# Kernel optimization log

Hardware: AMD Instinct MI355X
Metric: run time of the kernel (lower is better)

Reference implementation:

```python
import jax, jax.numpy as jnp
import numpy as np

N, E, D_IN, HID, HEADS, D_OUT, R = 20000, 640000, 256, 128, 4, 128, 32
NEG_SLOPE = 0.2  # PyG GATConv default


def setup_inputs() -> dict:
    key = jax.random.key(0)
    ks = jax.random.split(key, 12)
    s = 0.05
    return {
        "x": jax.random.normal(ks[0], (N, D_IN), jnp.float32),
        "edge_index": jax.random.randint(ks[1], (2, E), 0, N, dtype=jnp.int64),
        "edge_type": jax.random.randint(ks[2], (E,), 0, R, dtype=jnp.int64),
        "rel_emb": jax.random.normal(ks[3], (R, D_IN), jnp.float32) * s,
        "W1": jax.random.normal(ks[4], (D_IN, HEADS * HID), jnp.float32) * s,
        "att_src1": jax.random.normal(ks[5], (HEADS, HID), jnp.float32) * s,
        "att_dst1": jax.random.normal(ks[6], (HEADS, HID), jnp.float32) * s,
        "b1": jnp.zeros((HEADS * HID,), jnp.float32),
        "W2": jax.random.normal(ks[7], (HEADS * HID, D_OUT), jnp.float32) * s,
        "att_src2": jax.random.normal(ks[8], (1, D_OUT), jnp.float32) * s,
        "att_dst2": jax.random.normal(ks[9], (1, D_OUT), jnp.float32) * s,
        "b2": jnp.zeros((D_OUT,), jnp.float32),
    }


def _gat_conv(x, src, dst, W, a_src, a_dst, bias, heads, ch):
    """PyG GATConv (eval mode, self loops already in src/dst)."""
    n = x.shape[0]
    h = (x @ W).reshape(n, heads, ch)                      # [N,H,C]
    alpha_s = jnp.einsum('nhc,hc->nh', h, a_src)           # [N,H]
    alpha_d = jnp.einsum('nhc,hc->nh', h, a_dst)
    e = jax.nn.leaky_relu(alpha_s[src] + alpha_d[dst], NEG_SLOPE)  # [E,H]
    # segment softmax over incoming edges of each dst node
    m = jax.ops.segment_max(e, dst, num_segments=n)        # [N,H]
    p = jnp.exp(e - m[dst])
    denom = jax.ops.segment_sum(p, dst, num_segments=n)
    alpha = p / (denom[dst] + 1e-16)                       # [E,H]
    out = jax.ops.segment_sum(h[src] * alpha[:, :, None], dst, num_segments=n)
    return out.reshape(n, heads * ch) + bias


def reference(x, edge_index, edge_type, rel_emb, W1, att_src1, att_dst1, b1,
              W2, att_src2, att_dst2, b2):
    src, dst = edge_index[0], edge_index[1]
    # relational feature injection: x_mod[src] += rel_emb[edge_type]
    x_mod = x.at[src].add(rel_emb[edge_type])
    # GATConv adds self loops by default
    loop = jnp.arange(N, dtype=src.dtype)
    s2 = jnp.concatenate([src, loop])
    d2 = jnp.concatenate([dst, loop])
    h = _gat_conv(x_mod, s2, d2, W1, att_src1, att_dst1, b1, HEADS, HID)
    h = jax.nn.elu(h)
    return _gat_conv(h, s2, d2, W2, att_src2, att_dst2, b2, 1, D_OUT)
```

## Files before the change

### kernel.cpp

```cpp
#include <hip/hip_runtime.h>


#define D_IN   256
#define HID1   512
#define NHEADS 4
#define DOUT   128
#define NREL   32
#define NEG_SLOPE 0.2f
#define M_PAD  20096
#define NB     128

static __device__ __forceinline__ unsigned short f2b(float f) {
  union { float f; unsigned int i; } v; v.f = f;
  unsigned int x = v.i;
  return (unsigned short)((x + 0x7fffu + ((x >> 16) & 1u)) >> 16);
}
static __device__ __forceinline__ float lrelu(float x) {
  return x > 0.f ? x : NEG_SLOPE * x;
}

typedef __attribute__((ext_vector_type(8))) short bf16x8;
typedef __attribute__((ext_vector_type(4))) float f32x4;
typedef __attribute__((ext_vector_type(2))) float f32x2;

static __device__ __forceinline__ f32x2 up2(unsigned int u) {
  union { unsigned int i; float f; } lo, hi;
  lo.i = u << 16; hi.i = u & 0xffff0000u;
  f32x2 v; v.x = lo.f; v.y = hi.f; return v;
}
static __device__ __forceinline__ void pkfma(f32x2& a, f32x2 b, f32x2 c) {
  asm("v_pk_fma_f32 %0, %1, %2, %0" : "+v"(a) : "v"(b), "v"(c));
}
static __device__ __forceinline__ void accp(f32x2* acc, float w, uint4 r) {
  f32x2 wv = (f32x2)(w);
  pkfma(acc[0], wv, up2(r.x));
  pkfma(acc[1], wv, up2(r.y));
  pkfma(acc[2], wv, up2(r.z));
  pkfma(acc[3], wv, up2(r.w));
}

__global__ __launch_bounds__(256) void hist_prep_kernel(
    const int* __restrict__ src, const int* __restrict__ dst,
    const int* __restrict__ et, unsigned int* __restrict__ counts8,
    int* __restrict__ gtable, int E, int n, int cb,
    const float* __restrict__ W1, const float* __restrict__ W2,
    unsigned short* __restrict__ W1T, unsigned short* __restrict__ W2T,
    const float* __restrict__ att_s1, const float* __restrict__ att_d1,
    float* __restrict__ us4, float* __restrict__ ud4,
    const float* __restrict__ att_s2, const float* __restrict__ att_d2,
    float* __restrict__ vs, float* __restrict__ vd) {
  int b = blockIdx.x;
  int t = threadIdx.x;
  if (b < NB) {
    extern __shared__ int hist[];
    for (int i = t; i < n; i += 256) hist[i] = 0;
    __syncthreads();
    int per = (E + NB - 1) / NB;
    int e0 = b * per;
    int e1 = min(e0 + per, E);
    for (int e = e0 + t; e < e1; e += 256) {
      atomicAdd(&hist[dst[e]], 1);
      int s = src[e], r = et[e];
      atomicAdd(&counts8[(size_t)s * 8 + (r >> 2)], 1u << (8 * (r & 3)));
    }
    __syncthreads();
    for (int i = t; i < n; i += 256) gtable[(size_t)b * n + i] = hist[i];
  } else if (b < NB + cb) {
    int idx = (b - NB) * 256 + t;
    if (idx < D_IN * HID1) {
      int r = idx / HID1, c = idx % HID1;
      W1T[(size_t)c * D_IN + r] = f2b(W1[idx]);
    } else {
      int k = idx - D_IN * HID1;
      if (k < HID1 * DOUT) {
        int r = k / DOUT, c = k % DOUT;
        W2T[(size_t)c * HID1 + r] = f2b(W2[k]);
      }
    }
  } else if (b == NB + cb) {
    int k = t;
    float us[4] = {0.f, 0.f, 0.f, 0.f}, ud[4] = {0.f, 0.f, 0.f, 0.f};
    for (int h = 0; h < 4; ++h)
      for (int c = 0; c < 128; ++c) {
        float wv = W1[(size_t)k * HID1 + h * 128 + c];
        us[h] += wv * att_s1[h * 128 + c];
        ud[h] += wv * att_d1[h * 128 + c];
      }
    ((float4*)us4)[k] = make_float4(us[0], us[1], us[2], us[3]);
    ((float4*)ud4)[k] = make_float4(ud[0], ud[1], ud[2], ud[3]);
  } else {
#pragma unroll
    for (int rr = 0; rr < 2; ++rr) {
      int r = t * 2 + rr;
      float ss = 0.f, dd = 0.f;
      for (int c = 0; c < DOUT; ++c) {
        float wv = W2[(size_t)r * DOUT + c];
        ss += wv * att_s2[c];
        dd += wv * att_d2[c];
      }
      vs[r] = ss; vd[r] = dd;
    }
  }
}

__global__ void colsum_kernel(const int* __restrict__ gtable,
                              int* __restrict__ deg, int n) {
  int d = blockIdx.x * 256 + threadIdx.x;
  if (d >= n) return;
  int s = 0;
#pragma unroll 8
  for (int b = 0; b < NB; ++b) s += gtable[(size_t)b * n + d];
  deg[d] = s;
}

__global__ void scan_local(const int* __restrict__ in, int* __restrict__ out,
                           int* __restrict__ bsum, int n) {
  __shared__ int wsum[4];
  int t = threadIdx.x;
  int base = blockIdx.x * 1024 + t * 4;
  int v0 = (base + 0 < n) ? in[base + 0] : 0;
  int v1 = (base + 1 < n) ? in[base + 1] : 0;
  int v2 = (base + 2 < n) ? in[base + 2] : 0;
  int v3 = (base + 3 < n) ? in[base + 3] : 0;
  int s = v0 + v1 + v2 + v3;
  int lane = t & 63, w = t >> 6;
  int sc = s;
  for (int off = 1; off < 64; off <<= 1) {
    int u = __shfl_up(sc, off);
    if (lane >= off) sc += u;
  }
  if (lane == 63) wsum[w] = sc;
  __syncthreads();
  int woff = 0;
  for (int i = 0; i < w; ++i) woff += wsum[i];
  int excl = woff + sc - s;
  if (base + 0 < n) out[base + 0] = excl;
  if (base + 1 < n) out[base + 1] = excl + v0;
  if (base + 2 < n) out[base + 2] = excl + v0 + v1;
  if (base + 3 < n) out[base + 3] = excl + v0 + v1 + v2;
  if (t == 255) bsum[blockIdx.x] = woff + sc;
}

__global__ void scan_blocks(int* __restrict__ bsum, int nb,
                            int* __restrict__ offsets, int n) {
  int t = threadIdx.x;
  int v = (t < nb) ? bsum[t] : 0;
  int sc = v;
  for (int off = 1; off < 64; off <<= 1) {
    int u = __shfl_up(sc, off);
    if (t >= off) sc += u;
  }
  if (t < nb) bsum[t] = sc - v;
  if (t == nb - 1) offsets[n] = v;
}

__global__ void rebase_kernel(int* __restrict__ gtable,
                              const int* __restrict__ offsets,
                              const int* __restrict__ bsum, int n) {
  int d = blockIdx.x * 256 + threadIdx.x;
  if (d >= n) return;
  int run = offsets[d] + bsum[d >> 10];
#pragma unroll 8
  for (int b = 0; b < NB; ++b) {
    size_t idx = (size_t)b * n + d;
    int v = gtable[idx];
    gtable[idx] = run;
    run += v;
  }
}

__global__ __launch_bounds__(256) void scatter2_kernel(
    const int* __restrict__ src, const int* __restrict__ dst,
    const int* __restrict__ gtable, int* __restrict__ csr_src,
    uint2* __restrict__ wexp,
    const float* __restrict__ as1, const float* __restrict__ ad1,
    int E, int n) {
  extern __shared__ int cur[];
  int b = blockIdx.x;
  int t = threadIdx.x;
  for (int i = t; i < n; i += 256) cur[i] = gtable[(size_t)b * n + i];
  __syncthreads();
  int per = (E + NB - 1) / NB;
  int e0 = b * per;
  int e1 = min(e0 + per, E);
  for (int e = e0 + t; e < e1; e += 256) {
    int d = dst[e], s = src[e];
    int pos = atomicAdd(&cur[d], 1);
    csr_src[pos] = s;
    float4 av = ((const float4*)as1)[s];
    float4 dv = ((const float4*)ad1)[d];
    unsigned short h0 = f2b(__expf(lrelu(av.x + dv.x)));
    unsigned short h1 = f2b(__expf(lrelu(av.y + dv.y)));
    unsigned short h2 = f2b(__expf(lrelu(av.z + dv.z)));
    unsigned short h3 = f2b(__expf(lrelu(av.w + dv.w)));
    wexp[pos] = make_uint2((unsigned)h0 | ((unsigned)h1 << 16),
                           (unsigned)h2 | ((unsigned)h3 << 16));
  }
}

__global__ __launch_bounds__(256) void xmod_kernel(
    const float* __restrict__ x, const unsigned int* __restrict__ counts8,
    const float* __restrict__ rel, const float* __restrict__ us4,
    const float* __restrict__ ud4, unsigned short* __restrict__ x_modb,
    float* __restrict__ as1, float* __restrict__ ad1, int n_nodes) {
  int wv = threadIdx.x >> 6;
  int node = blockIdx.x * 4 + wv;
  if (node >= n_nodes) return;
  int l = threadIdx.x & 63;
  int r5 = l & 31;
  unsigned int cw = counts8[(size_t)node * 8 + (r5 >> 2)];
  int cnt_l = (int)((cw >> (8 * (r5 & 3))) & 0xffu);
  const float4* x4 = (const float4*)x;
  const float4* rel4 = (const float4*)rel;
  float4 v = x4[(size_t)node * 64 + l];
#pragma unroll
  for (int r = 0; r < NREL; ++r) {
    int c = __shfl(cnt_l, r);
    if (c) {
      float4 rv = rel4[r * 64 + l];
      float fc = (float)c;
      v.x += fc * rv.x; v.y += fc * rv.y; v.z += fc * rv.z; v.w += fc * rv.w;
    }
  }
  ushort4 o;
  o.x = f2b(v.x); o.y = f2b(v.y); o.z = f2b(v.z); o.w = f2b(v.w);
  *(ushort4*)(x_modb + (size_t)node * D_IN + l * 4) = o;
  const float4* usv = (const float4*)us4;
  const float4* udv = (const float4*)ud4;
  float vv[4] = {v.x, v.y, v.z, v.w};
  float sh[4] = {0.f, 0.f, 0.f, 0.f}, dh[4] = {0.f, 0.f, 0.f, 0.f};
#pragma unroll
  for (int i = 0; i < 4; ++i) {
    float4 uu = usv[l * 4 + i];
    float4 dd = udv[l * 4 + i];
    sh[0] += vv[i] * uu.x; sh[1] += vv[i] * uu.y; sh[2] += vv[i] * uu.z; sh[3] += vv[i] * uu.w;
    dh[0] += vv[i] * dd.x; dh[1] += vv[i] * dd.y; dh[2] += vv[i] * dd.z; dh[3] += vv[i] * dd.w;
  }
  for (int off = 32; off; off >>= 1) {
#pragma unroll
    for (int h = 0; h < 4; ++h) {
      sh[h] += __shfl_xor(sh[h], off);
      dh[h] += __shfl_xor(dh[h], off);
    }
  }
  if (l == 0) {
    ((float4*)as1)[node] = make_float4(sh[0], sh[1], sh[2], sh[3]);
    ((float4*)ad1)[node] = make_float4(dh[0], dh[1], dh[2], dh[3]);
  }
}

__global__ __launch_bounds__(256) void aggregate1_kernel(
    const unsigned short* __restrict__ x_modb,
    const uint2* __restrict__ wexp,
    const float* __restrict__ as1, const float* __restrict__ ad1,
    const int* __restrict__ offsets, const int* __restrict__ bsum,
    const int* __restrict__ csr_src,
    unsigned short* __restrict__ agg_xb, int n_nodes) {
  int node = blockIdx.x * 4 + (threadIdx.x >> 6);
  if (node >= n_nodes) return;
  int lane = threadIdx.x & 63;
  int half = lane >> 5, l32 = lane & 31;
  int lo = offsets[node] + bsum[node >> 10];
  int hi = offsets[node + 1] + bsum[(node + 1) >> 10];
  const uint4* xv = (const uint4*)x_modb;

  f32x2 acc[4][4];
#pragma unroll
  for (int h = 0; h < 4; ++h)
#pragma unroll
    for (int k = 0; k < 4; ++k) acc[h][k] = (f32x2)(0.f);
  f32x2 den01 = (f32x2)(0.f), den23 = (f32x2)(0.f);

  int j = lo + half;
  int s = (j < hi) ? csr_src[j] : node;
  uint2 w = (j < hi) ? wexp[j] : make_uint2(0u, 0u);
  uint4 r = xv[(unsigned)((s << 5) | l32)];
  while (j < hi) {
    int jn = j + 2;
    int sn = (jn < hi) ? csr_src[jn] : node;
    uint2 wn = (jn < hi) ? wexp[jn] : make_uint2(0u, 0u);
    uint4 rn = xv[(unsigned)((sn << 5) | l32)];
    f32x2 w01 = up2(w.x), w23 = up2(w.y);
    den01 += w01; den23 += w23;
    f32x2 x0 = up2(r.x), x1 = up2(r.y), x2 = up2(r.z), x3 = up2(r.w);
    f32x2 wv0 = (f32x2)(w01.x), wv1 = (f32x2)(w01.y);
    f32x2 wv2 = (f32x2)(w23.x), wv3 = (f32x2)(w23.y);
    pkfma(acc[0][0], wv0, x0); pkfma(acc[0][1], wv0, x1);
    pkfma(acc[0][2], wv0, x2); pkfma(acc[0][3], wv0, x3);
    pkfma(acc[1][0], wv1, x0); pkfma(acc[1][1], wv1, x1);
    pkfma(acc[1][2], wv1, x2); pkfma(acc[1][3], wv1, x3);
    pkfma(acc[2][0], wv2, x0); pkfma(acc[2][1], wv2, x1);
    pkfma(acc[2][2], wv2, x2); pkfma(acc[2][3], wv2, x3);
    pkfma(acc[3][0], wv3, x0); pkfma(acc[3][1], wv3, x1);
    pkfma(acc[3][2], wv3, x2); pkfma(acc[3][3], wv3, x3);
    j = jn; s = sn; w = wn; r = rn;
  }
  if (half == 0) {
    float4 av = ((const float4*)as1)[node];
    float4 dv = ((const float4*)ad1)[node];
    unsigned short h0 = f2b(__expf(lrelu(av.x + dv.x)));
    unsigned short h1 = f2b(__expf(lrelu(av.y + dv.y)));
    unsigned short h2 = f2b(__expf(lrelu(av.z + dv.z)));
    unsigned short h3 = f2b(__expf(lrelu(av.w + dv.w)));
    unsigned wlo = (unsigned)h0 | ((unsigned)h1 << 16);
    unsigned whi = (unsigned)h2 | ((unsigned)h3 << 16);
    f32x2 w01 = up2(wlo), w23 = up2(whi);
    den01 += w01; den23 += w23;
    uint4 rs = xv[(unsigned)((node << 5) | l32)];
    f32x2 x0 = up2(rs.x), x1 = up2(rs.y), x2 = up2(rs.z), x3 = up2(rs.w);
    f32x2 wv0 = (f32x2)(w01.x), wv1 = (f32x2)(w01.y);
    f32x2 wv2 = (f32x2)(w23.x), wv3 = (f32x2)(w23.y);
    pkfma(acc[0][0], wv0, x0); pkfma(acc[0][1], wv0, x1);
    pkfma(acc[0][2], wv0, x2); pkfma(acc[0][3], wv0, x3);
    pkfma(acc[1][0], wv1, x0); pkfma(acc[1][1], wv1, x1);
    pkfma(acc[1][2], wv1, x2); pkfma(acc[1][3], wv1, x3);
    pkfma(acc[2][0], wv2, x0); pkfma(acc[2][1], wv2, x1);
    pkfma(acc[2][2], wv2, x2); pkfma(acc[2][3], wv2, x3);
    pkfma(acc[3][0], wv3, x0); pkfma(acc[3][1], wv3, x1);
    pkfma(acc[3][2], wv3, x2); pkfma(acc[3][3], wv3, x3);
  }
#pragma unroll
  for (int h = 0; h < 4; ++h)
#pragma unroll
    for (int k = 0; k < 4; ++k) {
      acc[h][k].x += __shfl_xor(acc[h][k].x, 32);
      acc[h][k].y += __shfl_xor(acc[h][k].y, 32);
    }
  den01.x += __shfl_xor(den01.x, 32); den01.y += __shfl_xor(den01.y, 32);
  den23.x += __shfl_xor(den23.x, 32); den23.y += __shfl_xor(den23.y, 32);
  if (half == 0) {
    float inv[4];
    inv[0] = 1.f / (den01.x + 1e-16f);
    inv[1] = 1.f / (den01.y + 1e-16f);
    inv[2] = 1.f / (den23.x + 1e-16f);
    inv[3] = 1.f / (den23.y + 1e-16f);
#pragma unroll
    for (int h = 0; h < 4; ++h) {
      uint4 o;
      o.x = (unsigned)f2b(acc[h][0].x * inv[h]) | ((unsigned)f2b(acc[h][0].y * inv[h]) << 16);
      o.y = (unsigned)f2b(acc[h][1].x * inv[h]) | ((unsigned)f2b(acc[h][1].y * inv[h]) << 16);
      o.z = (unsigned)f2b(acc[h][2].x * inv[h]) | ((unsigned)f2b(acc[h][2].y * inv[h]) << 16);
      o.w = (unsigned)f2b(acc[h][3].x * inv[h]) | ((unsigned)f2b(acc[h][3].y * inv[h]) << 16);
      *(uint4*)(agg_xb + ((size_t)h * M_PAD + node) * D_IN + l32 * 8) = o;
    }
  }
}

template <int BM, int MODE>
__global__ __launch_bounds__(256) void mfma_gemm(
    const unsigned short* __restrict__ A, const unsigned short* __restrict__ BT,
    unsigned short* __restrict__ C, int M, int N, int K,
    const float* __restrict__ bias, const float* __restrict__ vs,
    const float* __restrict__ vd, float* __restrict__ as2, float* __restrict__ ad2) {
  constexpr int MFR = BM / 32;
  __shared__ __align__(16) unsigned short Asl[BM * 32];
  __shared__ __align__(16) unsigned short Bsl[128 * 32];
  int tid = threadIdx.x;
  int m0 = blockIdx.y * BM, n0 = blockIdx.x * 128;
  int lane = tid & 63, wv = tid >> 6;
  int wm = wv & 1, wn = wv >> 1;
  int l16 = lane & 15, quad = lane >> 4;
  int lr = lane >> 2, lseg = lane & 3;
  if (MODE == 1) A += (size_t)blockIdx.x * M_PAD * K;

  f32x4 acc[MFR][4];
#pragma unroll
  for (int i = 0; i < MFR; ++i)
#pragma unroll
    for (int j = 0; j < 4; ++j) acc[i][j] = (f32x4)(0.f);

  for (int k0 = 0; k0 < K; k0 += 32) {
#pragma unroll
    for (int c = wv; c < BM / 16; c += 4) {
      int gr = m0 + c * 16 + lr; gr = gr < M ? gr : M - 1;
      __builtin_amdgcn_global_load_lds(
          (const __attribute__((address_space(1))) void*)(A + (size_t)gr * K + k0 + lseg * 8),
          (__attribute__((address_space(3))) void*)(&Asl[c * 512]), 16, 0, 0);
    }
#pragma unroll
    for (int c = wv; c < 8; c += 4) {
      int gr = n0 + c * 16 + lr;
      __builtin_amdgcn_global_load_lds(
          (const __attribute__((address_space(1))) void*)(BT + (size_t)gr * K + k0 + lseg * 8),
          (__attribute__((address_space(3))) void*)(&Bsl[c * 512]), 16, 0, 0);
    }
    __syncthreads();
    bf16x8 af[MFR], bfr[4];
#pragma unroll
    for (int mf = 0; mf < MFR; ++mf)
      af[mf] = *(const bf16x8*)(&Asl[(wm * (BM / 2) + mf * 16 + l16) * 32 + quad * 8]);
#pragma unroll
    for (int nf = 0; nf < 4; ++nf)
      bfr[nf] = *(const bf16x8*)(&Bsl[(wn * 64 + nf * 16 + l16) * 32 + quad * 8]);
#pragma unroll
    for (int mf = 0; mf < MFR; ++mf)
#pragma unroll
      for (int nf = 0; nf < 4; ++nf)
        acc[mf][nf] = __builtin_amdgcn_mfma_f32_16x16x32_bf16(af[mf], bfr[nf], acc[mf][nf], 0, 0, 0);
    __syncthreads();
  }
  if (MODE == 0) {
#pragma unroll
    for (int mf = 0; mf < MFR; ++mf)
#pragma unroll
      for (int nf = 0; nf < 4; ++nf)
#pragma unroll
        for (int r = 0; r < 4; ++r) {
          int row = m0 + wm * (BM / 2) + mf * 16 + quad * 4 + r;
          int col = n0 + wn * 64 + nf * 16 + l16;
          C[(size_t)row * N + col] = f2b(acc[mf][nf][r]);
        }
  } else {
#pragma unroll
    for (int mf = 0; mf < MFR; ++mf)
#pragma unroll
      for (int r = 0; r < 4; ++r) {
        int row = m0 + wm * (BM / 2) + mf * 16 + quad * 4 + r;
        float sd = 0.f, dd = 0.f;
#pragma unroll
        for (int nf = 0; nf < 4; ++nf) {
          int col = n0 + wn * 64 + nf * 16 + l16;
          float cv = acc[mf][nf][r] + bias[col];
          cv = cv > 0.f ? cv : expm1f(cv);
          C[(size_t)row * N + col] = f2b(cv);
          sd += cv * vs[col];
          dd += cv * vd[col];
        }
#pragma unroll
        for (int off = 1; off < 16; off <<= 1) {
          sd += __shfl_xor(sd, off);
          dd += __shfl_xor(dd, off);
        }
        if (l16 == 0 && row < M) {
          atomicAdd(&as2[row], sd);
          atomicAdd(&ad2[row], dd);
        }
      }
  }
}

__global__ __launch_bounds__(256) void aggregate2_kernel(
    const unsigned short* __restrict__ t2b,
    const float* __restrict__ as2, const float* __restrict__ ad2,
    const int* __restrict__ offsets, const int* __restrict__ bsum,
    const int* __restrict__ csr_src,
    const float* __restrict__ bias, float* __restrict__ out, int n_nodes) {
  int node = blockIdx.x * 4 + (threadIdx.x >> 6);
  if (node >= n_nodes) return;
  int lane = threadIdx.x & 63;
  int g = lane >> 4, l16 = lane & 15;
  int lo = offsets[node] + bsum[node >> 10];
  int hi = offsets[node + 1] + bsum[(node + 1) >> 10];
  float ad = ad2[node];

  const uint4* t2v = (const uint4*)t2b;
  f32x2 acc[4];
#pragma unroll
  for (int k = 0; k < 4; ++k) acc[k] = (f32x2)(0.f);
  float denom = 0.f;
  int nit = (hi - lo + 3) >> 2;
  int j = lo + g;
  bool valid = j < hi;
  int s = valid ? csr_src[j] : node;
  float asv = as2[s];
  uint4 tv = t2v[(unsigned)((s << 4) | l16)];
  for (int i = 0; i < nit; ++i) {
    int jn = j + 4;
    bool vn = jn < hi;
    int sn = vn ? csr_src[jn] : node;
    float asv_n = as2[sn];
    uint4 tvn = t2v[(unsigned)((sn << 4) | l16)];
    float w = valid ? __expf(lrelu(asv + ad)) : 0.f;
    accp(acc, w, tv);
    denom += w;
    j = jn; valid = vn; s = sn; asv = asv_n; tv = tvn;
  }
  if (g == 0) {
    uint4 tv2 = t2v[(unsigned)((node << 4) | l16)];
    float w = __expf(lrelu(as2[node] + ad));
    accp(acc, w, tv2);
    denom += w;
  }
#pragma unroll
  for (int k = 0; k < 4; ++k) {
    acc[k].x += __shfl_xor(acc[k].x, 16); acc[k].y += __shfl_xor(acc[k].y, 16);
    acc[k].x += __shfl_xor(acc[k].x, 32); acc[k].y += __shfl_xor(acc[k].y, 32);
  }
  denom += __shfl_xor(denom, 16);
  denom += __shfl_xor(denom, 32);
  if (g == 0) {
    float inv = 1.f / (denom + 1e-16f);
    float4 o0, o1;
    o0.x = acc[0].x * inv + bias[l16 * 8 + 0];
    o0.y = acc[0].y * inv + bias[l16 * 8 + 1];
    o0.z = acc[1].x * inv + bias[l16 * 8 + 2];
    o0.w = acc[1].y * inv + bias[l16 * 8 + 3];
    o1.x = acc[2].x * inv + bias[l16 * 8 + 4];
    o1.y = acc[2].y * inv + bias[l16 * 8 + 5];
    o1.z = acc[3].x * inv + bias[l16 * 8 + 6];
    o1.w = acc[3].y * inv + bias[l16 * 8 + 7];
    *(float4*)(out + (size_t)node * DOUT + l16 * 8) = o0;
    *(float4*)(out + (size_t)node * DOUT + l16 * 8 + 4) = o1;
  }
}

extern "C" void kernel_launch(void* const* d_in, const int* in_sizes, int n_in,
                              void* d_out, int out_size, void* d_ws, size_t ws_size,
                              hipStream_t stream) {
  const float* x     = (const float*)d_in[0];
  const int* ei      = (const int*)d_in[1];
  const int* etype   = (const int*)d_in[2];
  const float* rel   = (const float*)d_in[3];
  const float* W1    = (const float*)d_in[4];
  const float* at_s1 = (const float*)d_in[5];
  const float* at_d1 = (const float*)d_in[6];
  const float* b1    = (const float*)d_in[7];
  const float* W2    = (const float*)d_in[8];
  const float* at_s2 = (const float*)d_in[9];
  const float* at_d2 = (const float*)d_in[10];
  const float* b2v   = (const float*)d_in[11];
  float* out         = (float*)d_out;

  const int N = in_sizes[0] / D_IN;
  const int E = in_sizes[2];
  const int* srcv = ei;
  const int* dstv = ei + E;

  char* p = (char*)d_ws;
  auto carve = [&](size_t bytes) -> char* {
    char* r = p; p += (bytes + 255) & ~(size_t)255; return r;
  };
  unsigned int* counts8 = (unsigned int*)carve((size_t)N * 8 * 4);
  float* as2     = (float*)carve((size_t)N * 4);
  float* ad2     = (float*)carve((size_t)N * 4);
  size_t zero_bytes = (size_t)(p - (char*)counts8);
  int*   deg     = (int*)carve((size_t)N * 4);
  int*   offsets = (int*)carve(((size_t)N + 1) * 4);
  int*   bsum    = (int*)carve(64 * 4);
  float* as1     = (float*)carve((size_t)N * NHEADS * 4);
  float* ad1     = (float*)carve((size_t)N * NHEADS * 4);
  float* vs      = (float*)carve((size_t)HID1 * 4);
  float* vd      = (float*)carve((size_t)HID1 * 4);
  float* us4     = (float*)carve((size_t)D_IN * 4 * 4);
  float* ud4     = (float*)carve((size_t)D_IN * 4 * 4);
  int*   csr_src = (int*)carve((size_t)E * 4);
  uint2* wexp    = (uint2*)carve((size_t)E * 8);
  unsigned short* W1T    = (unsigned short*)carve((size_t)HID1 * D_IN * 2);
  unsigned short* W2T    = (unsigned short*)carve((size_t)DOUT * HID1 * 2);
  unsigned short* x_modb = (unsigned short*)carve((size_t)N * D_IN * 2);
  unsigned short* agg_xb = (unsigned short*)carve((size_t)NHEADS * M_PAD * D_IN * 2);
  unsigned short* h2b    = (unsigned short*)carve((size_t)M_PAD * HID1 * 2);
  unsigned short* t2b    = (unsigned short*)carve((size_t)M_PAD * DOUT * 2);
  int* gtable = (int*)h2b;

  (void)hipMemsetAsync(counts8, 0, zero_bytes, stream);

  int cb = (D_IN * HID1 + HID1 * DOUT + 255) / 256;
  int nb = (N + 1023) / 1024;
  int ldsb = N * 4;
  hist_prep_kernel<<<NB + cb + 2, 256, ldsb, stream>>>(
      srcv, dstv, etype, counts8, gtable, E, N, cb,
      W1, W2, W1T, W2T, at_s1, at_d1, us4, ud4, at_s2, at_d2, vs, vd);
  colsum_kernel<<<(N + 255) / 256, 256, 0, stream>>>(gtable, deg, N);
  scan_local<<<nb, 256, 0, stream>>>(deg, offsets, bsum, N);
  scan_blocks<<<1, 64, 0, stream>>>(bsum, nb, offsets, N);
  rebase_kernel<<<(N + 255) / 256, 256, 0, stream>>>(gtable, offsets, bsum, N);
  xmod_kernel<<<(N + 3) / 4, 256, 0, stream>>>(x, counts8, rel, us4, ud4, x_modb, as1, ad1, N);
  scatter2_kernel<<<NB, 256, ldsb, stream>>>(srcv, dstv, gtable, csr_src, wexp,
                                             as1, ad1, E, N);
  aggregate1_kernel<<<(N + 3) / 4, 256, 0, stream>>>(x_modb, wexp, as1, ad1, offsets,
                                                     bsum, csr_src, agg_xb, N);
  mfma_gemm<128, 1><<<dim3(NHEADS, M_PAD / 128), 256, 0, stream>>>(
      agg_xb, W1T, h2b, N, HID1, D_IN, b1, vs, vd, as2, ad2);
  mfma_gemm<64, 0><<<dim3(DOUT / 128, M_PAD / 64), 256, 0, stream>>>(
      h2b, W2T, t2b, N, DOUT, HID1, nullptr, nullptr, nullptr, nullptr, nullptr);
  aggregate2_kernel<<<(N + 3) / 4, 256, 0, stream>>>(
      t2b, as2, ad2, offsets, bsum, csr_src, b2v, out, N);
}
```

Before: 309.2 us.

## Fuse colsum with xmod, single-block scan, parallelize prep dots, fp32 edge weights

Parallelizes the attention-vector precompute blocks across more blocks with vectorized loads and shuffle reduction. Merges the degree column-sum into the x_mod kernel launch and replaces the three-kernel scan with a single-block serial scan, which removes the bsum indirection from the aggregators. Edge softmax weights are stored as fp32 float4 instead of packed bf16, and aggregate1 is unrolled two edges deep using op_sel packed FMAs. The result is fewer launches and less unpacking, at the cost of doubled edge-weight traffic and a serial single-block scan over 20k entries.

```diff
diff --git a/kernel.cpp b/kernel.cpp
--- a/kernel.cpp
+++ b/kernel.cpp
@@ -31,12 +31,35 @@
 static __device__ __forceinline__ void pkfma(f32x2& a, f32x2 b, f32x2 c) {
   asm("v_pk_fma_f32 %0, %1, %2, %0" : "+v"(a) : "v"(b), "v"(c));
 }
+static __device__ __forceinline__ void pkfma_l(f32x2& a, f32x2 b, f32x2 c) {
+  asm("v_pk_fma_f32 %0, %1, %2, %0 op_sel_hi:[0,1,1]"
+      : "+v"(a) : "v"(b), "v"(c));
+}
+static __device__ __forceinline__ void pkfma_h(f32x2& a, f32x2 b, f32x2 c) {
+  asm("v_pk_fma_f32 %0, %1, %2, %0 op_sel:[1,0,0]"
+      : "+v"(a) : "v"(b), "v"(c));
+}
 static __device__ __forceinline__ void accp(f32x2* acc, float w, uint4 r) {
   f32x2 wv = (f32x2)(w);
   pkfma(acc[0], wv, up2(r.x));
   pkfma(acc[1], wv, up2(r.y));
   pkfma(acc[2], wv, up2(r.z));
   pkfma(acc[3], wv, up2(r.w));
+}
+static __device__ __forceinline__ void acc4w(f32x2 acc[4][4], f32x2& den01,
+                                             f32x2& den23, float4 w, uint4 r) {
+  f32x2 w01; w01.x = w.x; w01.y = w.y;
+  f32x2 w23; w23.x = w.z; w23.y = w.w;
+  den01 += w01; den23 += w23;
+  f32x2 x0 = up2(r.x), x1 = up2(r.y), x2 = up2(r.z), x3 = up2(r.w);
+  pkfma_l(acc[0][0], w01, x0); pkfma_l(acc[0][1], w01, x1);
+  pkfma_l(acc[0][2], w01, x2); pkfma_l(acc[0][3], w01, x3);
+  pkfma_h(acc[1][0], w01, x0); pkfma_h(acc[1][1], w01, x1);
+  pkfma_h(acc[1][2], w01, x2); pkfma_h(acc[1][3], w01, x3);
+  pkfma_l(acc[2][0], w23, x0); pkfma_l(acc[2][1], w23, x1);
+  pkfma_l(acc[2][2], w23, x2); pkfma_l(acc[2][3], w23, x3);
+  pkfma_h(acc[3][0], w23, x0); pkfma_h(acc[3][1], w23, x1);
+  pkfma_h(acc[3][2], w23, x2); pkfma_h(acc[3][3], w23, x3);
 }
 
 __global__ __launch_bounds__(256) void hist_prep_kernel(
@@ -77,90 +100,137 @@
         W2T[(size_t)c * HID1 + r] = f2b(W2[k]);
       }
     }
-  } else if (b == NB + cb) {
-    int k = t;
-    float us[4] = {0.f, 0.f, 0.f, 0.f}, ud[4] = {0.f, 0.f, 0.f, 0.f};
-    for (int h = 0; h < 4; ++h)
-      for (int c = 0; c < 128; ++c) {
-        float wv = W1[(size_t)k * HID1 + h * 128 + c];
-        us[h] += wv * att_s1[h * 128 + c];
-        ud[h] += wv * att_d1[h * 128 + c];
-      }
-    ((float4*)us4)[k] = make_float4(us[0], us[1], us[2], us[3]);
-    ((float4*)ud4)[k] = make_float4(ud[0], ud[1], ud[2], ud[3]);
+  } else if (b < NB + cb + 8) {
+    int k = (b - NB - cb) * 32 + (t >> 3);
+    int ch0 = (t & 7) * 64;
+    int h = (t & 7) >> 1;
+    const float4* w4 = (const float4*)(W1 + (size_t)k * HID1 + ch0);
+    const float4* s4 = (const float4*)(att_s1 + ch0);
+    const float4* d4 = (const float4*)(att_d1 + ch0);
+    float us = 0.f, ud = 0.f;
+#pragma unroll
+    for (int i = 0; i < 16; ++i) {
+      float4 wv = w4[i], sv = s4[i], dv = d4[i];
+      us += wv.x * sv.x + wv.y * sv.y + wv.z * sv.z + wv.w * sv.w;
+      ud += wv.x * dv.x + wv.y * dv.y + wv.z * dv.z + wv.w * dv.w;
+    }
+    us += __shfl_xor(us, 1);
+    ud += __shfl_xor(ud, 1);
+    if ((t & 1) == 0) { us4[k * 4 + h] = us; ud4[k * 4 + h] = ud; }
   } else {
-#pragma unroll
-    for (int rr = 0; rr < 2; ++rr) {
-      int r = t * 2 + rr;
-      float ss = 0.f, dd = 0.f;
-      for (int c = 0; c < DOUT; ++c) {
-        float wv = W2[(size_t)r * DOUT + c];
-        ss += wv * att_s2[c];
-        dd += wv * att_d2[c];
-      }
-      vs[r] = ss; vd[r] = dd;
-    }
-  }
-}
-
-__global__ void colsum_kernel(const int* __restrict__ gtable,
-                              int* __restrict__ deg, int n) {
+    int r = (b - NB - cb - 8) * 128 + (t >> 1);
+    int c0 = (t & 1) * 64;
+    const float4* w4 = (const float4*)(W2 + (size_t)r * DOUT + c0);
+    const float4* s4 = (const float4*)(att_s2 + c0);
+    const float4* d4 = (const float4*)(att_d2 + c0);
+    float ss = 0.f, dd = 0.f;
+#pragma unroll
+    for (int i = 0; i < 16; ++i) {
+      float4 wv = w4[i], sv = s4[i], dv = d4[i];
+      ss += wv.x * sv.x + wv.y * sv.y + wv.z * sv.z + wv.w * sv.w;
+      dd += wv.x * dv.x + wv.y * dv.y + wv.z * dv.z + wv.w * dv.w;
+    }
+    ss += __shfl_xor(ss, 1);
+    dd += __shfl_xor(dd, 1);
+    if ((t & 1) == 0) { vs[r] = ss; vd[r] = dd; }
+  }
+}
+
+__global__ __launch_bounds__(256) void colsum_xmod_kernel(
+    const int* __restrict__ gtable, int* __restrict__ offsets, int cs,
+    const float* __restrict__ x, const unsigned int* __restrict__ counts8,
+    const float* __restrict__ rel, const float* __restrict__ us4,
+    const float* __restrict__ ud4, unsigned short* __restrict__ x_modb,
+    float* __restrict__ as1, float* __restrict__ ad1, int n_nodes) {
+  int b = blockIdx.x;
+  int t = threadIdx.x;
+  if (b < cs) {
+    int d = b * 256 + t;
+    if (d >= n_nodes) return;
+    int s = 0;
+    for (int bb = 0; bb < NB; ++bb) s += gtable[(size_t)bb * n_nodes + d];
+    offsets[d] = s;
+    return;
+  }
+  int wv = t >> 6;
+  int node = (b - cs) * 4 + wv;
+  if (node >= n_nodes) return;
+  int l = t & 63;
+  int r5 = l & 31;
+  unsigned int cw = counts8[(size_t)node * 8 + (r5 >> 2)];
+  int cnt_l = (int)((cw >> (8 * (r5 & 3))) & 0xffu);
+  const float4* x4 = (const float4*)x;
+  const float4* rel4 = (const float4*)rel;
+  float4 v = x4[(size_t)node * 64 + l];
+#pragma unroll
+  for (int r = 0; r < NREL; ++r) {
+    int c = __shfl(cnt_l, r);
+    if (c) {
+      float4 rv = rel4[r * 64 + l];
+      float fc = (float)c;
+      v.x += fc * rv.x; v.y += fc * rv.y; v.z += fc * rv.z; v.w += fc * rv.w;
+    }
+  }
+  ushort4 o;
+  o.x = f2b(v.x); o.y = f2b(v.y); o.z = f2b(v.z); o.w = f2b(v.w);
+  *(ushort4*)(x_modb + (size_t)node * D_IN + l * 4) = o;
+  const float4* usv = (const float4*)us4;
+  const float4* udv = (const float4*)ud4;
+  float vv[4] = {v.x, v.y, v.z, v.w};
+  float sh[4] = {0.f, 0.f, 0.f, 0.f}, dh[4] = {0.f, 0.f, 0.f, 0.f};
+#pragma unroll
+  for (int i = 0; i < 4; ++i) {
+    float4 uu = usv[l * 4 + i];
+    float4 dd = udv[l * 4 + i];
+    sh[0] += vv[i] * uu.x; sh[1] += vv[i] * uu.y; sh[2] += vv[i] * uu.z; sh[3] += vv[i] * uu.w;
+    dh[0] += vv[i] * dd.x; dh[1] += vv[i] * dd.y; dh[2] += vv[i] * dd.z; dh[3] += vv[i] * dd.w;
+  }
+  for (int off = 32; off; off >>= 1) {
+#pragma unroll
+    for (int h = 0; h < 4; ++h) {
+      sh[h] += __shfl_xor(sh[h], off);
+      dh[h] += __shfl_xor(dh[h], off);
+    }
+  }
+  if (l == 0) {
+    ((float4*)as1)[node] = make_float4(sh[0], sh[1], sh[2], sh[3]);
+    ((float4*)ad1)[node] = make_float4(dh[0], dh[1], dh[2], dh[3]);
+  }
+}
+
+__global__ __launch_bounds__(256) void scan_full_kernel(int* __restrict__ offsets,
+                                                        int n) {
+  __shared__ int wsum[4];
+  __shared__ int carry;
+  int t = threadIdx.x;
+  int lane = t & 63, w = t >> 6;
+  if (t == 0) carry = 0;
+  __syncthreads();
+  for (int base = 0; base < n; base += 256) {
+    int i = base + t;
+    int v = (i < n) ? offsets[i] : 0;
+    int sc = v;
+    for (int off = 1; off < 64; off <<= 1) {
+      int u = __shfl_up(sc, off);
+      if (lane >= off) sc += u;
+    }
+    if (lane == 63) wsum[w] = sc;
+    __syncthreads();
+    int woff = carry;
+    for (int k = 0; k < w; ++k) woff += wsum[k];
+    if (i < n) offsets[i] = woff + sc - v;
+    __syncthreads();
+    if (t == 255) carry = woff + sc;
+    __syncthreads();
+  }
+  if (t == 0) offsets[n] = carry;
+}
+
+__global__ void rebase_kernel(int* __restrict__ gtable,
+                              const int* __restrict__ offsets, int n) {
   int d = blockIdx.x * 256 + threadIdx.x;
   if (d >= n) return;
-  int s = 0;
-#pragma unroll 8
-  for (int b = 0; b < NB; ++b) s += gtable[(size_t)b * n + d];
-  deg[d] = s;
-}
-
-__global__ void scan_local(const int* __restrict__ in, int* __restrict__ out,
-                           int* __restrict__ bsum, int n) {
-  __shared__ int wsum[4];
-  int t = threadIdx.x;
-  int base = blockIdx.x * 1024 + t * 4;
-  int v0 = (base + 0 < n) ? in[base + 0] : 0;
-  int v1 = (base + 1 < n) ? in[base + 1] : 0;
-  int v2 = (base + 2 < n) ? in[base + 2] : 0;
-  int v3 = (base + 3 < n) ? in[base + 3] : 0;
-  int s = v0 + v1 + v2 + v3;
-  int lane = t & 63, w = t >> 6;
-  int sc = s;
-  for (int off = 1; off < 64; off <<= 1) {
-    int u = __shfl_up(sc, off);
-    if (lane >= off) sc += u;
-  }
-  if (lane == 63) wsum[w] = sc;
-  __syncthreads();
-  int woff = 0;
-  for (int i = 0; i < w; ++i) woff += wsum[i];
-  int excl = woff + sc - s;
-  if (base + 0 < n) out[base + 0] = excl;
-  if (base + 1 < n) out[base + 1] = excl + v0;
-  if (base + 2 < n) out[base + 2] = excl + v0 + v1;
-  if (base + 3 < n) out[base + 3] = excl + v0 + v1 + v2;
-  if (t == 255) bsum[blockIdx.x] = woff + sc;
-}
-
-__global__ void scan_blocks(int* __restrict__ bsum, int nb,
-                            int* __restrict__ offsets, int n) {
-  int t = threadIdx.x;
-  int v = (t < nb) ? bsum[t] : 0;
-  int sc = v;
-  for (int off = 1; off < 64; off <<= 1) {
-    int u = __shfl_up(sc, off);
-    if (t >= off) sc += u;
-  }
-  if (t < nb) bsum[t] = sc - v;
-  if (t == nb - 1) offsets[n] = v;
-}
-
-__global__ void rebase_kernel(int* __restrict__ gtable,
-                              const int* __restrict__ offsets,
-                              const int* __restrict__ bsum, int n) {
-  int d = blockIdx.x * 256 + threadIdx.x;
-  if (d >= n) return;
-  int run = offsets[d] + bsum[d >> 10];
-#pragma unroll 8
+  int run = offsets[d];
   for (int b = 0; b < NB; ++b) {
     size_t idx = (size_t)b * n + d;
     int v = gtable[idx];
@@ -172,7 +242,7 @@
 __global__ __launch_bounds__(256) void scatter2_kernel(
     const int* __restrict__ src, const int* __restrict__ dst,
     const int* __restrict__ gtable, int* __restrict__ csr_src,
-    uint2* __restrict__ wexp,
+    float4* __restrict__ wexp,
     const float* __restrict__ as1, const float* __restrict__ ad1,
     int E, int n) {
   extern __shared__ int cur[];
@@ -189,80 +259,26 @@
     csr_src[pos] = s;
     float4 av = ((const float4*)as1)[s];
     float4 dv = ((const float4*)ad1)[d];
-    unsigned short h0 = f2b(__expf(lrelu(av.x + dv.x)));
-    unsigned short h1 = f2b(__expf(lrelu(av.y + dv.y)));
-    unsigned short h2 = f2b(__expf(lrelu(av.z + dv.z)));
-    unsigned short h3 = f2b(__expf(lrelu(av.w + dv.w)));
-    wexp[pos] = make_uint2((unsigned)h0 | ((unsigned)h1 << 16),
-                           (unsigned)h2 | ((unsigned)h3 << 16));
-  }
-}
-
-__global__ __launch_bounds__(256) void xmod_kernel(
-    const float* __restrict__ x, const unsigned int* __restrict__ counts8,
-    const float* __restrict__ rel, const float* __restrict__ us4,
-    const float* __restrict__ ud4, unsigned short* __restrict__ x_modb,
-    float* __restrict__ as1, float* __restrict__ ad1, int n_nodes) {
-  int wv = threadIdx.x >> 6;
-  int node = blockIdx.x * 4 + wv;
-  if (node >= n_nodes) return;
-  int l = threadIdx.x & 63;
-  int r5 = l & 31;
-  unsigned int cw = counts8[(size_t)node * 8 + (r5 >> 2)];
-  int cnt_l = (int)((cw >> (8 * (r5 & 3))) & 0xffu);
-  const float4* x4 = (const float4*)x;
-  const float4* rel4 = (const float4*)rel;
-  float4 v = x4[(size_t)node * 64 + l];
-#pragma unroll
-  for (int r = 0; r < NREL; ++r) {
-    int c = __shfl(cnt_l, r);
-    if (c) {
-      float4 rv = rel4[r * 64 + l];
-      float fc = (float)c;
-      v.x += fc * rv.x; v.y += fc * rv.y; v.z += fc * rv.z; v.w += fc * rv.w;
-    }
-  }
-  ushort4 o;
-  o.x = f2b(v.x); o.y = f2b(v.y); o.z = f2b(v.z); o.w = f2b(v.w);
-  *(ushort4*)(x_modb + (size_t)node * D_IN + l * 4) = o;
-  const float4* usv = (const float4*)us4;
-  const float4* udv = (const float4*)ud4;
-  float vv[4] = {v.x, v.y, v.z, v.w};
-  float sh[4] = {0.f, 0.f, 0.f, 0.f}, dh[4] = {0.f, 0.f, 0.f, 0.f};
-#pragma unroll
-  for (int i = 0; i < 4; ++i) {
-    float4 uu = usv[l * 4 + i];
-    float4 dd = udv[l * 4 + i];
-    sh[0] += vv[i] * uu.x; sh[1] += vv[i] * uu.y; sh[2] += vv[i] * uu.z; sh[3] += vv[i] * uu.w;
-    dh[0] += vv[i] * dd.x; dh[1] += vv[i] * dd.y; dh[2] += vv[i] * dd.z; dh[3] += vv[i] * dd.w;
-  }
-  for (int off = 32; off; off >>= 1) {
-#pragma unroll
-    for (int h = 0; h < 4; ++h) {
-      sh[h] += __shfl_xor(sh[h], off);
-      dh[h] += __shfl_xor(dh[h], off);
-    }
-  }
-  if (l == 0) {
-    ((float4*)as1)[node] = make_float4(sh[0], sh[1], sh[2], sh[3]);
-    ((float4*)ad1)[node] = make_float4(dh[0], dh[1], dh[2], dh[3]);
+    wexp[pos] = make_float4(__expf(lrelu(av.x + dv.x)),
+                            __expf(lrelu(av.y + dv.y)),
+                            __expf(lrelu(av.z + dv.z)),
+                            __expf(lrelu(av.w + dv.w)));
   }
 }
 
 __global__ __launch_bounds__(256) void aggregate1_kernel(
     const unsigned short* __restrict__ x_modb,
-    const uint2* __restrict__ wexp,
+    const float4* __restrict__ wexp,
     const float* __restrict__ as1, const float* __restrict__ ad1,
-    const int* __restrict__ offsets, const int* __restrict__ bsum,
-    const int* __restrict__ csr_src,
+    const int* __restrict__ offsets, const int* __restrict__ csr_src,
     unsigned short* __restrict__ agg_xb, int n_nodes) {
   int node = blockIdx.x * 4 + (threadIdx.x >> 6);
   if (node >= n_nodes) return;
   int lane = threadIdx.x & 63;
   int half = lane >> 5, l32 = lane & 31;
-  int lo = offsets[node] + bsum[node >> 10];
-  int hi = offsets[node + 1] + bsum[(node + 1) >> 10];
+  int lo = offsets[node], hi = offsets[node + 1];
   const uint4* xv = (const uint4*)x_modb;
+  const float4 z4 = make_float4(0.f, 0.f, 0.f, 0.f);
 
   f32x2 acc[4][4];
 #pragma unroll
@@ -272,52 +288,35 @@
   f32x2 den01 = (f32x2)(0.f), den23 = (f32x2)(0.f);
 
   int j = lo + half;
-  int s = (j < hi) ? csr_src[j] : node;
-  uint2 w = (j < hi) ? wexp[j] : make_uint2(0u, 0u);
-  uint4 r = xv[(unsigned)((s << 5) | l32)];
+  int s0 = (j < hi) ? csr_src[j] : node;
+  float4 wA = (j < hi) ? wexp[j] : z4;
+  uint4 rA = xv[(unsigned)((s0 << 5) | l32)];
+  int j1 = j + 2;
+  int s1 = (j1 < hi) ? csr_src[j1] : node;
+  float4 wB = (j1 < hi) ? wexp[j1] : z4;
+  uint4 rB = xv[(unsigned)((s1 << 5) | l32)];
   while (j < hi) {
-    int jn = j + 2;
-    int sn = (jn < hi) ? csr_src[jn] : node;
-    uint2 wn = (jn < hi) ? wexp[jn] : make_uint2(0u, 0u);
-    uint4 rn = xv[(unsigned)((sn << 5) | l32)];
-    f32x2 w01 = up2(w.x), w23 = up2(w.y);
-    den01 += w01; den23 += w23;
-    f32x2 x0 = up2(r.x), x1 = up2(r.y), x2 = up2(r.z), x3 = up2(r.w);
-    f32x2 wv0 = (f32x2)(w01.x), wv1 = (f32x2)(w01.y);
-    f32x2 wv2 = (f32x2)(w23.x), wv3 = (f32x2)(w23.y);
-    pkfma(acc[0][0], wv0, x0); pkfma(acc[0][1], wv0, x1);
-    pkfma(acc[0][2], wv0, x2); pkfma(acc[0][3], wv0, x3);
-    pkfma(acc[1][0], wv1, x0); pkfma(acc[1][1], wv1, x1);
-    pkfma(acc[1][2], wv1, x2); pkfma(acc[1][3], wv1, x3);
-    pkfma(acc[2][0], wv2, x0); pkfma(acc[2][1], wv2, x1);
-    pkfma(acc[2][2], wv2, x2); pkfma(acc[2][3], wv2, x3);
-    pkfma(acc[3][0], wv3, x0); pkfma(acc[3][1], wv3, x1);
-    pkfma(acc[3][2], wv3, x2); pkfma(acc[3][3], wv3, x3);
-    j = jn; s = sn; w = wn; r = rn;
+    int jA = j + 4;
+    int sA = (jA < hi) ? csr_src[jA] : node;
+    float4 wAn = (jA < hi) ? wexp[jA] : z4;
+    uint4 rAn = xv[(unsigned)((sA << 5) | l32)];
+    acc4w(acc, den01, den23, wA, rA);
+    int jB = j + 6;
+    int sB = (jB < hi) ? csr_src[jB] : node;
+    float4 wBn = (jB < hi) ? wexp[jB] : z4;
+    uint4 rBn = xv[(unsigned)((sB << 5) | l32)];
+    acc4w(acc, den01, den23, wB, rB);
+    j = jA; wA = wAn; rA = rAn; wB = wBn; rB = rBn;
   }
   if (half == 0) {
     float4 av = ((const float4*)as1)[node];
     float4 dv = ((const float4*)ad1)[node];
-    unsigned short h0 = f2b(__expf(lrelu(av.x + dv.x)));
-    unsigned short h1 = f2b(__expf(lrelu(av.y + dv.y)));
-    unsigned short h2 = f2b(__expf(lrelu(av.z + dv.z)));
-    unsigned short h3 = f2b(__expf(lrelu(av.w + dv.w)));
-    unsigned wlo = (unsigned)h0 | ((unsigned)h1 << 16);
-    unsigned whi = (unsigned)h2 | ((unsigned)h3 << 16);
-    f32x2 w01 = up2(wlo), w23 = up2(whi);
-    den01 += w01; den23 += w23;
+    float4 sw = make_float4(__expf(lrelu(av.x + dv.x)),
+                            __expf(lrelu(av.y + dv.y)),
+                            __expf(lrelu(av.z + dv.z)),
+                            __expf(lrelu(av.w + dv.w)));
     uint4 rs = xv[(unsigned)((node << 5) | l32)];
-    f32x2 x0 = up2(rs.x), x1 = up2(rs.y), x2 = up2(rs.z), x3 = up2(rs.w);
-    f32x2 wv0 = (f32x2)(w01.x), wv1 = (f32x2)(w01.y);
-    f32x2 wv2 = (f32x2)(w23.x), wv3 = (f32x2)(w23.y);
-    pkfma(acc[0][0], wv0, x0); pkfma(acc[0][1], wv0, x1);
-    pkfma(acc[0][2], wv0, x2); pkfma(acc[0][3], wv0, x3);
-    pkfma(acc[1][0], wv1, x0); pkfma(acc[1][1], wv1, x1);
-    pkfma(acc[1][2], wv1, x2); pkfma(acc[1][3], wv1, x3);
-    pkfma(acc[2][0], wv2, x0); pkfma(acc[2][1], wv2, x1);
-    pkfma(acc[2][2], wv2, x2); pkfma(acc[2][3], wv2, x3);
-    pkfma(acc[3][0], wv3, x0); pkfma(acc[3][1], wv3, x1);
-    pkfma(acc[3][2], wv3, x2); pkfma(acc[3][3], wv3, x3);
+    acc4w(acc, den01, den23, sw, rs);
   }
 #pragma unroll
   for (int h = 0; h < 4; ++h)
@@ -442,15 +441,13 @@
 __global__ __launch_bounds__(256) void aggregate2_kernel(
     const unsigned short* __restrict__ t2b,
     const float* __restrict__ as2, const float* __restrict__ ad2,
-    const int* __restrict__ offsets, const int* __restrict__ bsum,
-    const int* __restrict__ csr_src,
+    const int* __restrict__ offsets, const int* __restrict__ csr_src,
     const float* __restrict__ bias, float* __restrict__ out, int n_nodes) {
   int node = blockIdx.x * 4 + (threadIdx.x >> 6);
   if (node >= n_nodes) return;
   int lane = threadIdx.x & 63;
   int g = lane >> 4, l16 = lane & 15;
-  int lo = offsets[node] + bsum[node >> 10];
-  int hi = offsets[node + 1] + bsum[(node + 1) >> 10];
+  int lo = offsets[node], hi = offsets[node + 1];
   float ad = ad2[node];
 
   const uint4* t2v = (const uint4*)t2b;
@@ -534,9 +531,7 @@
   float* as2     = (float*)carve((size_t)N * 4);
   float* ad2     = (float*)carve((size_t)N * 4);
   size_t zero_bytes = (size_t)(p - (char*)counts8);
-  int*   deg     = (int*)carve((size_t)N * 4);
   int*   offsets = (int*)carve(((size_t)N + 1) * 4);
-  int*   bsum    = (int*)carve(64 * 4);
   float* as1     = (float*)carve((size_t)N * NHEADS * 4);
   float* ad1     = (float*)carve((size_t)N * NHEADS * 4);
   float* vs      = (float*)carve((size_t)HID1 * 4);
@@ -544,7 +539,7 @@
   float* us4     = (float*)carve((size_t)D_IN * 4 * 4);
   float* ud4     = (float*)carve((size_t)D_IN * 4 * 4);
   int*   csr_src = (int*)carve((size_t)E * 4);
-  uint2* wexp    = (uint2*)carve((size_t)E * 8);
+  float4* wexp   = (float4*)carve((size_t)E * 16);
   unsigned short* W1T    = (unsigned short*)carve((size_t)HID1 * D_IN * 2);
   unsigned short* W2T    = (unsigned short*)carve((size_t)DOUT * HID1 * 2);
   unsigned short* x_modb = (unsigned short*)carve((size_t)N * D_IN * 2);
@@ -556,24 +551,24 @@
   (void)hipMemsetAsync(counts8, 0, zero_bytes, stream);
 
   int cb = (D_IN * HID1 + HID1 * DOUT + 255) / 256;
-  int nb = (N + 1023) / 1024;
+  int cs = (N + 255) / 256;
+  int xb = (N + 3) / 4;
   int ldsb = N * 4;
-  hist_prep_kernel<<<NB + cb + 2, 256, ldsb, stream>>>(
+  hist_prep_kernel<<<NB + cb + 12, 256, ldsb, stream>>>(
       srcv, dstv, etype, counts8, gtable, E, N, cb,
       W1, W2, W1T, W2T, at_s1, at_d1, us4, ud4, at_s2, at_d2, vs, vd);
-  colsum_kernel<<<(N + 255) / 256, 256, 0, stream>>>(gtable, deg, N);
-  scan_local<<<nb, 256, 0, stream>>>(deg, offsets, bsum, N);
-  scan_blocks<<<1, 64, 0, stream>>>(bsum, nb, offsets, N);
-  rebase_kernel<<<(N + 255) / 256, 256, 0, stream>>>(gtable, offsets, bsum, N);
-  xmod_kernel<<<(N + 3) / 4, 256, 0, stream>>>(x, counts8, rel, us4, ud4, x_modb, as1, ad1, N);
+  colsum_xmod_kernel<<<cs + xb, 256, 0, stream>>>(
+      gtable, offsets, cs, x, counts8, rel, us4, ud4, x_modb, as1, ad1, N);
+  scan_full_kernel<<<1, 256, 0, stream>>>(offsets, N);
+  rebase_kernel<<<cs, 256, 0, stream>>>(gtable, offsets, N);
   scatter2_kernel<<<NB, 256, ldsb, stream>>>(srcv, dstv, gtable, csr_src, wexp,
                                              as1, ad1, E, N);
-  aggregate1_kernel<<<(N + 3) / 4, 256, 0, stream>>>(x_modb, wexp, as1, ad1, offsets,
-                                                     bsum, csr_src, agg_xb, N);
+  aggregate1_kernel<<<xb, 256, 0, stream>>>(x_modb, wexp, as1, ad1, offsets,
+                                            csr_src, agg_xb, N);
   mfma_gemm<128, 1><<<dim3(NHEADS, M_PAD / 128), 256, 0, stream>>>(
       agg_xb, W1T, h2b, N, HID1, D_IN, b1, vs, vd, as2, ad2);
   mfma_gemm<64, 0><<<dim3(DOUT / 128, M_PAD / 64), 256, 0, stream>>>(
       h2b, W2T, t2b, N, DOUT, HID1, nullptr, nullptr, nullptr, nullptr, nullptr);
-  aggregate2_kernel<<<(N + 3) / 4, 256, 0, stream>>>(
-      t2b, as2, ad2, offsets, bsum, csr_src, b2v, out, N);
-}
+  aggregate2_kernel<<<xb, 256, 0, stream>>>(
+      t2b, as2, ad2, offsets, csr_src, b2v, out, N);
+}
```

Result: slower. 363.4 us (+17.5%).
